# Kernel optimization log

Hardware: AMD Instinct MI355X
Metric: run time of the kernel (lower is better)

## Reference

```python
import jax, jax.numpy as jnp
import numpy as np

E = 512   # embed_dim
H = 8     # num_heads
B = 64    # num graphs
N = 255   # nodes per graph (equal counts -> padded mask is all-true)


def setup_inputs() -> dict:
    key = jax.random.key(0)
    ks = jax.random.split(key, 12)
    x = jax.random.normal(ks[0], (B * N, E), jnp.float32)
    metal_x = jax.random.normal(ks[1], (B, E), jnp.float32)
    batch = jnp.repeat(jnp.arange(B, dtype=jnp.int32), N)
    s = 1.0 / np.sqrt(E)
    def u(k, shape):
        return jax.random.uniform(k, shape, jnp.float32, -s, s)
    return {
        "x": x, "metal_x": metal_x, "batch": batch,
        "Wq": u(ks[2], (E, E)), "Wk": u(ks[3], (E, E)), "Wv": u(ks[4], (E, E)),
        "bq": u(ks[5], (E,)), "bk": u(ks[6], (E,)), "bv": u(ks[7], (E,)),
        "Wo": u(ks[8], (E, E)), "bo": u(ks[9], (E,)),
    }


def reference(x, metal_x, batch, Wq, Wk, Wv, bq, bk, bv, Wo, bo):
    # batch is sorted with equal per-graph counts, so the torch
    # pad_sequence([cat(metal_x[i], x[batch==i])]) construction is exactly a
    # reshape + concat, and key_padding_mask (~mask) is all-False.
    nb, e = metal_x.shape
    n = x.shape[0] // nb
    L = n + 1
    dh = e // H
    # value: [B, L, E] with the metal token at position 0
    value = jnp.concatenate([metal_x[:, None, :], x.reshape(nb, n, e)], axis=1)
    # key/query_sequential are identity; torch MHA in-projections (y = x W^T + b)
    q = value @ Wq.T + bq
    k = value @ Wk.T + bk
    v = value @ Wv.T + bv
    def heads(t):  # [B, L, E] -> [B, H, L, Dh]
        return t.reshape(nb, L, H, dh).transpose(0, 2, 1, 3)
    qh, kh, vh = heads(q), heads(k), heads(v)
    scale = 1.0 / jnp.sqrt(jnp.asarray(dh, q.dtype))
    scores = jnp.einsum('bhld,bhmd->bhlm', qh, kh) * scale
    attn = jax.nn.softmax(scores, axis=-1)
    oh = jnp.einsum('bhlm,bhmd->bhld', attn, vh)          # [B, H, L, Dh]
    out = oh.transpose(0, 2, 1, 3).reshape(nb, L, e) @ Wo.T + bo  # [B, L, E]
    # torch output is [L, B, E]; boolean indexing out[x_mask.T] iterates
    # row-major over (l, b): all graphs at node slot 1, then slot 2, ...
    out_lb = out.transpose(1, 0, 2)                        # [L, B, E]
    x_out = out_lb[1:].reshape(nb * n, e)
    metal_x_out = out_lb[0]                                # [B, E]
    return x_out, metal_x_out
```

## Files before the change

kernel.cpp:

```cpp
#include <hip/hip_runtime.h>
#include <stdint.h>


#define EMB    512
#define NH     8
#define NGR    64
#define SEQL   256
#define DHEAD  64
#define MROWS  16384

typedef __attribute__((ext_vector_type(4))) float f32x4;
typedef __attribute__((ext_vector_type(4))) short s16x4;
typedef __attribute__((ext_vector_type(8))) short s16x8;

__device__ __forceinline__ short f2bf(float f) {
  uint32_t u = __builtin_bit_cast(uint32_t, f);
  u += 0x7FFFu + ((u >> 16) & 1u);
  return (short)(u >> 16);
}

__device__ __forceinline__ f32x4 mfma16(s16x8 a, s16x8 b, f32x4 c) {
  return __builtin_amdgcn_mfma_f32_16x16x32_bf16(a, b, c, 0, 0, 0);
}

__device__ __forceinline__ void gload_lds16(const void* g, void* l) {
  __builtin_amdgcn_global_load_lds(
      (const __attribute__((address_space(1))) void*)g,
      (__attribute__((address_space(3))) void*)l, 16, 0, 0);
}


__global__ void pack_value(const float* __restrict__ x, const float* __restrict__ mx,
                           short* __restrict__ val) {
  int gid = blockIdx.x * 256 + threadIdx.x;
  int i = gid << 2;
  int row = i >> 9, col = i & 511;
  int b = row >> 8, l = row & 255;
  const float* src = l ? x  + ((size_t)(b * 255 + l - 1) << 9) + col
                       : mx + ((size_t)b << 9) + col;
  f32x4 f = *(const f32x4*)src;
  s16x4 o = { f2bf(f[0]), f2bf(f[1]), f2bf(f[2]), f2bf(f[3]) };
  *(s16x4*)(val + i) = o;
}

__global__ void pack_w(const float* __restrict__ Wq, const float* __restrict__ Wk,
                       const float* __restrict__ Wv, const float* __restrict__ Wo,
                       const float* __restrict__ bq, const float* __restrict__ bk,
                       const float* __restrict__ bv,
                       short* __restrict__ wqkv, short* __restrict__ wo,
                       float* __restrict__ bias_qkv) {
  int gid = blockIdx.x * 256 + threadIdx.x;
  int i = gid << 2;
  const float* src; short* dst;
  if (i < 786432) {
    int which = i >> 18, off = i & 262143;
    src = (which == 0 ? Wq : which == 1 ? Wk : Wv) + off;
    dst = wqkv + i;
  } else {
    int off = i - 786432;
    src = Wo + off; dst = wo + off;
  }
  f32x4 f = *(const f32x4*)src;
  s16x4 o = { f2bf(f[0]), f2bf(f[1]), f2bf(f[2]), f2bf(f[3]) };
  *(s16x4*)dst = o;
  if (gid < 1536)
    bias_qkv[gid] = gid < 512 ? bq[gid] : gid < 1024 ? bk[gid - 512] : bv[gid - 1024];
}

#define BM 128
#define BN 128
#define BK 32

__global__ __launch_bounds__(256, 2) void gemm_bt(
    const short* __restrict__ A, const short* __restrict__ Bt,
    const float* __restrict__ bias, int mode,
    short* __restrict__ qb, short* __restrict__ kb, short* __restrict__ vb,
    float* __restrict__ outp) {
  __shared__ short As[2][BM * BK];
  __shared__ short Bs[2][BN * BK];
  const int tid = threadIdx.x;
  const int lane = tid & 63, wid = tid >> 6;
  const int wr = wid >> 1, wc = wid & 1;
  const int l15 = lane & 15, l4 = lane >> 4;
  const int bm = blockIdx.x * BM, bn = blockIdx.y * BN;

  f32x4 acc[4][4];
#pragma unroll
  for (int r = 0; r < 4; ++r)
#pragma unroll
    for (int c = 0; c < 4; ++c) acc[r][c] = (f32x4){0.f, 0.f, 0.f, 0.f};

#pragma unroll
  for (int i = 0; i < 2; ++i) {
    int idx = i * 256 + tid;
    int row = idx >> 2, cc = (idx & 3) * 8;
    gload_lds16(A + (size_t)(bm + row) * 512 + cc, &As[0][idx * 8]);
    gload_lds16(Bt + (size_t)(bn + row) * 512 + cc, &Bs[0][idx * 8]);
  }
  __syncthreads();

  int cur = 0;
  for (int t = 0; t < 512 / BK; ++t) {
    if (t < 512 / BK - 1) {
      const int bk = (t + 1) * BK;
#pragma unroll
      for (int i = 0; i < 2; ++i) {
        int idx = i * 256 + tid;
        int row = idx >> 2, cc = (idx & 3) * 8;
        gload_lds16(A + (size_t)(bm + row) * 512 + bk + cc, &As[cur ^ 1][idx * 8]);
        gload_lds16(Bt + (size_t)(bn + row) * 512 + bk + cc, &Bs[cur ^ 1][idx * 8]);
      }
    }

    s16x8 af[4], bf[4];
#pragma unroll
    for (int r = 0; r < 4; ++r)
      af[r] = *(const s16x8*)(&As[cur][(wr * 64 + r * 16 + l15) * BK + l4 * 8]);
#pragma unroll
    for (int c = 0; c < 4; ++c)
      bf[c] = *(const s16x8*)(&Bs[cur][(wc * 64 + c * 16 + l15) * BK + l4 * 8]);
#pragma unroll
    for (int r = 0; r < 4; ++r)
#pragma unroll
      for (int c = 0; c < 4; ++c)
        acc[r][c] = mfma16(af[r], bf[c], acc[r][c]);

    __syncthreads();
    cur ^= 1;
  }

#pragma unroll
  for (int r = 0; r < 4; ++r) {
    int row0 = bm + wr * 64 + r * 16 + l4 * 4;
#pragma unroll
    for (int c = 0; c < 4; ++c) {
      int col_g = bn + wc * 64 + c * 16 + l15;
      float bvv = bias[col_g];
#pragma unroll
      for (int j = 0; j < 4; ++j) {
        float v = acc[r][c][j] + bvv;
        int row = row0 + j;
        int b = row >> 8, lrow = row & 255;
        if (mode == 0) {
          int which = col_g >> 9, rem = col_g & 511;
          int h = rem >> 6, dh = rem & 63;
          size_t idx = ((size_t)((b * 8 + h) * 256 + lrow)) * 64 + dh;
          (which == 0 ? qb : which == 1 ? kb : vb)[idx] = f2bf(v);
        } else {
          size_t idx = (lrow == 0)
                         ? (size_t)16320 * 512 + (size_t)b * 512 + col_g
                         : ((size_t)(lrow - 1) * 64 + b) * 512 + col_g;
          outp[idx] = v;
        }
      }
    }
  }
}

#define VT_ROWB 544

__global__ __launch_bounds__(256, 2) void attn(
    const short* __restrict__ qb, const short* __restrict__ kb,
    const short* __restrict__ vb, short* __restrict__ attn_out) {
  __shared__ short Kl[256 * 64];
  __shared__ short VT[64 * 272];
  __shared__ short Pl[4][16 * 72];

  const int tid = threadIdx.x;
  const int lane = tid & 63, w = tid >> 6;
  const int l15 = lane & 15, l4 = lane >> 4;
  const int hb = blockIdx.x;
  const int bh = (hb & 7) * 64 + ((hb >> 3) >> 2);
  const int quarter = (hb >> 3) & 3;
  const size_t base = (size_t)bh * SEQL * DHEAD;

  {
    const char* kbytes = (const char*)(kb + base);
#pragma unroll
    for (int c = 0; c < 8; ++c) {
      int o = c * 4096 + tid * 16;
      int src = o ^ (((o >> 7) & 7) << 4);
      gload_lds16(kbytes + src, (char*)Kl + o);
    }
  }

  {
    int d0 = (tid & 7) * 8;
    int krow = tid >> 3;
#pragma unroll
    for (int step = 0; step < 8; ++step) {
      int key = step * 32 + krow;
      s16x8 vv = *(const s16x8*)(vb + base + (size_t)key * 64 + d0);
#pragma unroll
      for (int j = 0; j < 8; ++j) {
        int d = d0 + j;
        int off = d * VT_ROWB + ((key * 2) ^ ((d << 1) & 0x70));
        *(short*)((char*)VT + off) = vv[j];
      }
    }
  }

  const int q0 = quarter * 64 + w * 16;
  s16x8 qf[2];
#pragma unroll
  for (int kk = 0; kk < 2; ++kk)
    qf[kk] = *(const s16x8*)(qb + base + (size_t)(q0 + l15) * 64 + kk * 32 + l4 * 8);

  __syncthreads();

  f32x4 s[16];
#pragma unroll
  for (int ct = 0; ct < 16; ++ct) s[ct] = (f32x4){0.f, 0.f, 0.f, 0.f};

#pragma unroll
  for (int ct = 0; ct < 16; ++ct) {
    int rawb = (ct * 16 + l15) * 128 + l4 * 16;
    int swz = (l15 & 7) << 4;
    s16x8 kf0 = *(const s16x8*)((const char*)Kl + (rawb ^ swz));
    s16x8 kf1 = *(const s16x8*)((const char*)Kl + ((rawb + 64) ^ swz));
    s[ct] = mfma16(qf[0], kf0, s[ct]);
    s[ct] = mfma16(qf[1], kf1, s[ct]);
  }

  const float scale = 0.125f;
  float lsum[4];
#pragma unroll
  for (int j = 0; j < 4; ++j) {
    float m = -1e30f;
#pragma unroll
    for (int ct = 0; ct < 16; ++ct) m = fmaxf(m, s[ct][j]);
#pragma unroll
    for (int d = 1; d < 16; d <<= 1) m = fmaxf(m, __shfl_xor(m, d, 64));
    m *= scale;
    float ls = 0.f;
#pragma unroll
    for (int ct = 0; ct < 16; ++ct) {
      float p = __expf(s[ct][j] * scale - m);
      s[ct][j] = p;
      ls += p;
    }
#pragma unroll
    for (int d = 1; d < 16; d <<= 1) ls += __shfl_xor(ls, d, 64);
    lsum[j] = ls;
  }

  f32x4 o[4];
#pragma unroll
  for (int jt = 0; jt < 4; ++jt) o[jt] = (f32x4){0.f, 0.f, 0.f, 0.f};

#pragma unroll
  for (int ck = 0; ck < 4; ++ck) {
#pragma unroll
    for (int c2 = 0; c2 < 4; ++c2)
#pragma unroll
      for (int j = 0; j < 4; ++j) {
        int q = l4 * 4 + j;
        int col = c2 * 16 + l15;
        Pl[w][q * 72 + col] = f2bf(s[ck * 4 + c2][j]);
      }
#pragma unroll
    for (int kk = 0; kk < 2; ++kk) {
      s16x8 pf = *(const s16x8*)(&Pl[w][l15 * 72 + kk * 32 + l4 * 8]);
#pragma unroll
      for (int jt = 0; jt < 4; ++jt) {
        int d = jt * 16 + l15;
        int k0 = ck * 64 + kk * 32 + l4 * 8;
        int off = d * VT_ROWB + ((k0 * 2) ^ ((d << 1) & 0x70));
        s16x8 vf = *(const s16x8*)((const char*)VT + off);
        o[jt] = mfma16(pf, vf, o[jt]);
      }
    }
  }

  const int b = bh >> 3, h = bh & 7;
#pragma unroll
  for (int jt = 0; jt < 4; ++jt)
#pragma unroll
    for (int j = 0; j < 4; ++j) {
      float val = o[jt][j] / lsum[j];
      int qrow = q0 + l4 * 4 + j;
      int d = jt * 16 + l15;
      attn_out[(size_t)(b * 256 + qrow) * 512 + h * 64 + d] = f2bf(val);
    }
}


extern "C" void kernel_launch(void* const* d_in, const int* in_sizes, int n_in,
                              void* d_out, int out_size, void* d_ws, size_t ws_size,
                              hipStream_t stream) {
  (void)in_sizes; (void)n_in; (void)out_size; (void)ws_size;
  const float* x  = (const float*)d_in[0];
  const float* mx = (const float*)d_in[1];
  const float* Wq = (const float*)d_in[3];
  const float* Wk = (const float*)d_in[4];
  const float* Wv = (const float*)d_in[5];
  const float* bq = (const float*)d_in[6];
  const float* bk = (const float*)d_in[7];
  const float* bv = (const float*)d_in[8];
  const float* Wo = (const float*)d_in[9];
  const float* bo = (const float*)d_in[10];
  float* out = (float*)d_out;

  char* ws = (char*)d_ws;
  short* value = (short*)(ws);
  short* wqkv  = (short*)(ws + 16777216);
  short* wo    = (short*)(ws + 18350080);
  float* biasq = (float*)(ws + 18874368);
  short* qbuf  = (short*)(ws + 18880512);
  short* kbuf  = (short*)(ws + 35657728);
  short* vbuf  = (short*)(ws + 52434944);
  short* attn_o = value;

  pack_value<<<8192, 256, 0, stream>>>(x, mx, value);
  pack_w<<<1024, 256, 0, stream>>>(Wq, Wk, Wv, Wo, bq, bk, bv, wqkv, wo, biasq);
  gemm_bt<<<dim3(128, 12), 256, 0, stream>>>(value, wqkv, biasq, 0,
                                             qbuf, kbuf, vbuf, nullptr);
  attn<<<2048, 256, 0, stream>>>(qbuf, kbuf, vbuf, attn_o);
  gemm_bt<<<dim3(128, 4), 256, 0, stream>>>(attn_o, wo, bo, 1,
                                            nullptr, nullptr, nullptr, out);
}
```

Measured before the change: 187.6 us.

## Triple-buffer GEMM LDS staging with one barrier per K-step

The bf16 GEMM moves from a double-buffered K loop with a trailing __syncthreads to a three-slot LDS ring. Tiles are prefetched two steps ahead, and an explicit s_waitcnt vmcnt(4) plus a single s_barrier waits only for the current tile's asynchronous loads. The aim is to keep more global-to-LDS traffic in flight behind the MFMA work and to drop one barrier per iteration. In exchange, LDS use per block rises by half, which could limit occupancy, and correctness now depends on a hand-counted vmcnt value that matches four loads per stage.

After: 184.5 us. Within noise of the previous version (-1.7%).

```diff
diff --git a/kernel.cpp b/kernel.cpp
--- a/kernel.cpp
+++ b/kernel.cpp
@@ -70,64 +70,70 @@
 #define BM 128
 #define BN 128
 #define BK 32
+#define NT 16
 
 __global__ __launch_bounds__(256, 2) void gemm_bt(
     const short* __restrict__ A, const short* __restrict__ Bt,
     const float* __restrict__ bias, int mode,
     short* __restrict__ qb, short* __restrict__ kb, short* __restrict__ vb,
     float* __restrict__ outp) {
-  __shared__ short As[2][BM * BK];
-  __shared__ short Bs[2][BN * BK];
+  __shared__ short As[3][BM * BK];
+  __shared__ short Bs[3][BN * BK];
   const int tid = threadIdx.x;
   const int lane = tid & 63, wid = tid >> 6;
   const int wr = wid >> 1, wc = wid & 1;
   const int l15 = lane & 15, l4 = lane >> 4;
   const int bm = blockIdx.x * BM, bn = blockIdx.y * BN;
 
+  auto STAGE = [&](int t, int b) {
+    const int bk = t * BK;
+#pragma unroll
+    for (int i = 0; i < 2; ++i) {
+      int idx = i * 256 + tid;
+      int row = idx >> 2, cc = (idx & 3) * 8;
+      gload_lds16(A + (size_t)(bm + row) * 512 + bk + cc, &As[b][idx * 8]);
+      gload_lds16(Bt + (size_t)(bn + row) * 512 + bk + cc, &Bs[b][idx * 8]);
+    }
+  };
+
   f32x4 acc[4][4];
 #pragma unroll
   for (int r = 0; r < 4; ++r)
 #pragma unroll
     for (int c = 0; c < 4; ++c) acc[r][c] = (f32x4){0.f, 0.f, 0.f, 0.f};
 
-#pragma unroll
-  for (int i = 0; i < 2; ++i) {
-    int idx = i * 256 + tid;
-    int row = idx >> 2, cc = (idx & 3) * 8;
-    gload_lds16(A + (size_t)(bm + row) * 512 + cc, &As[0][idx * 8]);
-    gload_lds16(Bt + (size_t)(bn + row) * 512 + cc, &Bs[0][idx * 8]);
-  }
-  __syncthreads();
-
-  int cur = 0;
-  for (int t = 0; t < 512 / BK; ++t) {
-    if (t < 512 / BK - 1) {
-      const int bk = (t + 1) * BK;
-#pragma unroll
-      for (int i = 0; i < 2; ++i) {
-        int idx = i * 256 + tid;
-        int row = idx >> 2, cc = (idx & 3) * 8;
-        gload_lds16(A + (size_t)(bm + row) * 512 + bk + cc, &As[cur ^ 1][idx * 8]);
-        gload_lds16(Bt + (size_t)(bn + row) * 512 + bk + cc, &Bs[cur ^ 1][idx * 8]);
-      }
-    }
-
+  auto COMPUTE = [&](int b) {
     s16x8 af[4], bf[4];
 #pragma unroll
     for (int r = 0; r < 4; ++r)
-      af[r] = *(const s16x8*)(&As[cur][(wr * 64 + r * 16 + l15) * BK + l4 * 8]);
+      af[r] = *(const s16x8*)(&As[b][(wr * 64 + r * 16 + l15) * BK + l4 * 8]);
 #pragma unroll
     for (int c = 0; c < 4; ++c)
-      bf[c] = *(const s16x8*)(&Bs[cur][(wc * 64 + c * 16 + l15) * BK + l4 * 8]);
+      bf[c] = *(const s16x8*)(&Bs[b][(wc * 64 + c * 16 + l15) * BK + l4 * 8]);
 #pragma unroll
     for (int r = 0; r < 4; ++r)
 #pragma unroll
       for (int c = 0; c < 4; ++c)
         acc[r][c] = mfma16(af[r], bf[c], acc[r][c]);
-
-    __syncthreads();
-    cur ^= 1;
-  }
+  };
+
+  STAGE(0, 0);
+  STAGE(1, 1);
+
+  int cur = 0;
+  for (int t = 0; t < NT - 1; ++t) {
+    asm volatile("s_waitcnt vmcnt(4) lgkmcnt(0)" ::: "memory");
+    __builtin_amdgcn_s_barrier();
+    if (t < NT - 2) {
+      int b2 = cur + 2; if (b2 >= 3) b2 -= 3;
+      STAGE(t + 2, b2);
+    }
+    COMPUTE(cur);
+    if (++cur == 3) cur = 0;
+  }
+  asm volatile("s_waitcnt vmcnt(0) lgkmcnt(0)" ::: "memory");
+  __builtin_amdgcn_s_barrier();
+  COMPUTE(cur);
 
 #pragma unroll
   for (int r = 0; r < 4; ++r) {
```
